# Kernel optimization log

Measured on AMD Instinct MI355X. Metric: run time of the kernel, lower is better.

Reference implementation:

```python
import jax, jax.numpy as jnp
import numpy as np
from jax import lax

B, P, DIM, HEADS, K = 2, 4096, 256, 8, 32
DH = DIM // HEADS
SCALE = DH ** -0.5


def setup_inputs() -> dict:
    key = jax.random.key(0)
    ks = jax.random.split(key, 12)
    s = 0.02
    return {
        "xyz": jax.random.uniform(ks[0], (B, P, 3), dtype=jnp.float32),
        "feats": jax.random.normal(ks[1], (B, P, DIM), dtype=jnp.float32),
        "Wq": jax.random.normal(ks[2], (DIM, DIM), dtype=jnp.float32) * s,
        "Wk": jax.random.normal(ks[3], (DIM, DIM), dtype=jnp.float32) * s,
        "Wv": jax.random.normal(ks[4], (DIM, DIM), dtype=jnp.float32) * s,
        "Wp": jax.random.normal(ks[5], (DIM, DIM), dtype=jnp.float32) * s,
        "bp": jnp.zeros((DIM,), jnp.float32),
        "W1": jax.random.normal(ks[6], (DIM, 3), dtype=jnp.float32) * s,
        "b1": jnp.zeros((DIM,), jnp.float32),
        "W2": jax.random.normal(ks[7], (DIM, DIM), dtype=jnp.float32) * s,
        "b2": jnp.zeros((DIM,), jnp.float32),
    }


def _gather(points, idx):
    # points: (B,N,C), idx: (B,M,K) -> (B,M,K,C)
    return jax.vmap(lambda p, i: p[i])(points, idx)


def reference(xyz, feats, Wq, Wk, Wv, Wp, bp, W1, b1, W2, b2):
    b, p, d = feats.shape
    # kNN via squared euclidean distance (same ordering as cdist)
    d2 = jnp.sum((xyz[:, :, None, :] - xyz[:, None, :, :]) ** 2, axis=-1)  # (B,P,P)
    _, idx = lax.top_k(-d2, K)  # (B,P,K) smallest distances

    neigh_xyz = _gather(xyz, idx)                      # (B,P,K,3)
    relpos = neigh_xyz - xyz[:, :, None, :]            # (B,P,K,3)

    q = (feats @ Wq.T).reshape(b, p, HEADS, DH)        # (B,P,H,Dh)
    k_full = feats @ Wk.T                              # (B,P,D)
    v_full = feats @ Wv.T
    k_nei = _gather(k_full, idx).reshape(b, p, K, HEADS, DH)
    v_nei = _gather(v_full, idx).reshape(b, p, K, HEADS, DH)

    # pos MLP: Linear(3,dim) -> ReLU -> Linear(dim,dim)
    h = jax.nn.relu(relpos @ W1.T + b1)
    pos_bias = (h @ W2.T + b2).reshape(b, p, K, HEADS, DH)

    attn = jnp.einsum('bphd,bpkhd->bpkh', q, k_nei + pos_bias) * SCALE
    attn = jax.nn.softmax(attn, axis=2)                # over K neighbors
    out = jnp.einsum('bpkh,bpkhd->bphd', attn, v_nei + pos_bias).reshape(b, p, d)
    return out @ Wp.T + bp
```

## Files before the change

### kernel.cpp

```cpp
#include <hip/hip_runtime.h>
#include <cstddef>

#define PB 4096
static constexpr float SCALE_F = 0.17677669529663687f;

typedef __attribute__((ext_vector_type(8))) short bf16x8;
typedef __attribute__((ext_vector_type(4))) float f32x4;

static __device__ __forceinline__ unsigned short f2bf(float x) {
  unsigned u = __builtin_bit_cast(unsigned, x);
  u += 0x7fffu + ((u >> 16) & 1u);
  return (unsigned short)(u >> 16);
}
static __device__ __forceinline__ float bf2f(unsigned short h) {
  return __builtin_bit_cast(float, (unsigned)h << 16);
}

__global__ __launch_bounds__(64) void knn_kernel(const float* __restrict__ xyz,
                                                 int* __restrict__ idx_out) {
  const int g = blockIdx.x;
  const int b = g >> 12;
  const int p = g & (PB - 1);
  const int lane = threadIdx.x;
  const float* base = xyz + (size_t)b * PB * 3;
  const float qx = base[p * 3 + 0];
  const float qy = base[p * 3 + 1];
  const float qz = base[p * 3 + 2];
  float list_d = 3.4e38f;
  int list_i = -1;
  for (int c = 0; c < PB / 64; ++c) {
    const int j = (c << 6) + lane;
    const float dx = __fsub_rn(qx, base[j * 3 + 0]);
    const float dy = __fsub_rn(qy, base[j * 3 + 1]);
    const float dz = __fsub_rn(qz, base[j * 3 + 2]);
    const float d2 = __fadd_rn(__fadd_rn(__fmul_rn(dx, dx), __fmul_rn(dy, dy)),
                               __fmul_rn(dz, dz));
    float worst = __shfl(list_d, 31);
    unsigned long long mask = __ballot(d2 < worst);
    while (mask) {
      const int l = __ffsll(mask) - 1;
      mask &= mask - 1;
      const float v = __shfl(d2, l);
      worst = __shfl(list_d, 31);
      if (v < worst) {
        const unsigned long long gt = __ballot((lane < 32) && (list_d > v));
        const int pos = __ffsll(gt) - 1;
        const float pd = __shfl_up(list_d, 1);
        const int pi = __shfl_up(list_i, 1);
        if (lane < 32 && lane >= pos) {
          const bool at = (lane == pos);
          list_d = at ? v : pd;
          list_i = at ? ((c << 6) + l) : pi;
        }
      }
    }
  }
  if (lane < 32) idx_out[(size_t)g * 32 + lane] = list_i;
}

__global__ __launch_bounds__(256) void prep_w(
    const float* __restrict__ Wq, const float* __restrict__ Wk,
    const float* __restrict__ Wv, const float* __restrict__ W2,
    const float* __restrict__ Wp,
    unsigned short* __restrict__ whi, unsigned short* __restrict__ wlo) {
  const int e = blockIdx.x * 256 + threadIdx.x;
  const int m = e >> 16;
  const int off = e & 65535;
  const float* src = (m == 0) ? Wq : (m == 1) ? Wk : (m == 2) ? Wv
                     : (m == 3) ? W2 : Wp;
  const float x = src[off];
  const unsigned short hi = f2bf(x);
  whi[e] = hi;
  wlo[e] = f2bf(x - bf2f(hi));
}

static __device__ __forceinline__ void gemm32_core(
    const float* __restrict__ A, const unsigned short* __restrict__ wh,
    const unsigned short* __restrict__ wl, const int r0,
    unsigned short* ah, unsigned short* al, f32x4 acc[2][4]) {
  const int tid = threadIdx.x;
#pragma unroll
  for (int t = 0; t < 8; ++t) {
    const int idx4 = (t << 8) + tid;
    const int row = idx4 >> 6;
    const int c4 = idx4 & 63;
    const float4 v = *(const float4*)(A + (size_t)(r0 + row) * 256 + (c4 << 2));
    const unsigned short h0 = f2bf(v.x), h1 = f2bf(v.y);
    const unsigned short h2 = f2bf(v.z), h3 = f2bf(v.w);
    const unsigned short l0 = f2bf(v.x - bf2f(h0)), l1 = f2bf(v.y - bf2f(h1));
    const unsigned short l2 = f2bf(v.z - bf2f(h2)), l3 = f2bf(v.w - bf2f(h3));
    const int base = (row << 9) + ((c4 << 3) ^ ((row & 7) << 4));
    *(uint2*)((char*)ah + base) =
        make_uint2((unsigned)h0 | ((unsigned)h1 << 16),
                   (unsigned)h2 | ((unsigned)h3 << 16));
    *(uint2*)((char*)al + base) =
        make_uint2((unsigned)l0 | ((unsigned)l1 << 16),
                   (unsigned)l2 | ((unsigned)l3 << 16));
  }
  __syncthreads();
  const int lane = tid & 63;
  const int w = tid >> 6;
  const int il = lane & 15;
  const int q4 = lane >> 4;
#pragma unroll
  for (int mt = 0; mt < 2; ++mt)
#pragma unroll
    for (int nt = 0; nt < 4; ++nt) acc[mt][nt] = (f32x4){0.f, 0.f, 0.f, 0.f};
#pragma unroll 2
  for (int ks = 0; ks < 8; ++ks) {
    bf16x8 bh[4], bl[4], a0[2], a1[2];
#pragma unroll
    for (int nt = 0; nt < 4; ++nt) {
      const int n = (w << 6) + (nt << 4) + il;
      const size_t off = (size_t)n * 256 + (ks << 5) + (q4 << 3);
      bh[nt] = *(const bf16x8*)(wh + off);
      bl[nt] = *(const bf16x8*)(wl + off);
    }
#pragma unroll
    for (int mt = 0; mt < 2; ++mt) {
      const int row = (mt << 4) + il;
      const int byte = (row << 9) + ((((ks << 5) + (q4 << 3)) << 1) ^ ((row & 7) << 4));
      a0[mt] = *(const bf16x8*)((const char*)ah + byte);
      a1[mt] = *(const bf16x8*)((const char*)al + byte);
    }
#pragma unroll
    for (int mt = 0; mt < 2; ++mt)
#pragma unroll
      for (int nt = 0; nt < 4; ++nt) {
        acc[mt][nt] = __builtin_amdgcn_mfma_f32_16x16x32_bf16(a0[mt], bh[nt], acc[mt][nt], 0, 0, 0);
        acc[mt][nt] = __builtin_amdgcn_mfma_f32_16x16x32_bf16(a1[mt], bh[nt], acc[mt][nt], 0, 0, 0);
        acc[mt][nt] = __builtin_amdgcn_mfma_f32_16x16x32_bf16(a0[mt], bl[nt], acc[mt][nt], 0, 0, 0);
      }
  }
}

__global__ __launch_bounds__(256) void qkv_mfma(
    const float* __restrict__ feats,
    const unsigned short* __restrict__ whi, const unsigned short* __restrict__ wlo,
    float* __restrict__ qb, unsigned short* __restrict__ kb16,
    unsigned short* __restrict__ vb16) {
  __shared__ unsigned short ah[32 * 256];
  __shared__ unsigned short al[32 * 256];
  const int bid = blockIdx.x;
  const int sel = bid % 3;
  const int r0 = (bid / 3) << 5;
  const unsigned short* wh = whi + (size_t)sel * 65536;
  const unsigned short* wl = wlo + (size_t)sel * 65536;
  f32x4 acc[2][4];
  gemm32_core(feats, wh, wl, r0, ah, al, acc);
  const int tid = threadIdx.x;
  const int lane = tid & 63;
  const int w = tid >> 6;
  const int il = lane & 15;
  const int q4 = lane >> 4;
#pragma unroll
  for (int mt = 0; mt < 2; ++mt)
#pragma unroll
    for (int nt = 0; nt < 4; ++nt) {
      const int col = (w << 6) + (nt << 4) + il;
#pragma unroll
      for (int r = 0; r < 4; ++r) {
        const size_t e = (size_t)(r0 + (mt << 4) + (q4 << 2) + r) * 256 + col;
        if (sel == 0) qb[e] = acc[mt][nt][r];
        else if (sel == 1) kb16[e] = f2bf(acc[mt][nt][r]);
        else vb16[e] = f2bf(acc[mt][nt][r]);
      }
    }
}

__global__ __launch_bounds__(256) void proj_mfma(
    const float* __restrict__ A,
    const unsigned short* __restrict__ whi, const unsigned short* __restrict__ wlo,
    const float* __restrict__ bp, float* __restrict__ C) {
  __shared__ unsigned short ah[32 * 256];
  __shared__ unsigned short al[32 * 256];
  const int r0 = blockIdx.x << 5;
  f32x4 acc[2][4];
  gemm32_core(A, whi, wlo, r0, ah, al, acc);
  const int tid = threadIdx.x;
  const int lane = tid & 63;
  const int w = tid >> 6;
  const int il = lane & 15;
  const int q4 = lane >> 4;
#pragma unroll
  for (int mt = 0; mt < 2; ++mt)
#pragma unroll
    for (int nt = 0; nt < 4; ++nt) {
      const int col = (w << 6) + (nt << 4) + il;
      const float bv = bp[col];
#pragma unroll
      for (int r = 0; r < 4; ++r)
        C[(size_t)(r0 + (mt << 4) + (q4 << 2) + r) * 256 + col] = acc[mt][nt][r] + bv;
    }
}

__global__ __launch_bounds__(256) void fused_kernel(
    const float* __restrict__ xyz, const int* __restrict__ nbr_idx,
    const float* __restrict__ qbuf, const unsigned short* __restrict__ kb16,
    const unsigned short* __restrict__ vb16,
    const float* __restrict__ W1, const float* __restrict__ b1,
    const unsigned short* __restrict__ w2bf, const float* __restrict__ b2,
    float* __restrict__ o_pre) {
  __shared__ unsigned short h_lds[32 * 256];
  __shared__ float q_lds[256];
  __shared__ float u_lds[8][256];
  __shared__ float c_lds[8][256];
  __shared__ float at_lds[32][8];
  __shared__ float rel[32][3];
  __shared__ int nbr_s[32];

  const int g = blockIdx.x;
  const int b = g >> 12;
  const int p = g & (PB - 1);
  const int tid = threadIdx.x;

  if (tid < 32) {
    const int j = nbr_idx[(size_t)g * 32 + tid];
    nbr_s[tid] = j;
    const float* xb = xyz + (size_t)b * PB * 3;
    rel[tid][0] = xb[j * 3 + 0] - xb[p * 3 + 0];
    rel[tid][1] = xb[j * 3 + 1] - xb[p * 3 + 1];
    rel[tid][2] = xb[j * 3 + 2] - xb[p * 3 + 2];
  }
  q_lds[tid] = qbuf[(size_t)g * 256 + tid];
  __syncthreads();

  {
    const int half = tid >> 7;
    const int c0 = (tid & 127) << 1;
    const float w00 = W1[c0 * 3 + 0], w01 = W1[c0 * 3 + 1], w02 = W1[c0 * 3 + 2];
    const float w10 = W1[c0 * 3 + 3], w11 = W1[c0 * 3 + 4], w12 = W1[c0 * 3 + 5];
    const float bb0 = b1[c0], bb1 = b1[c0 + 1];
#pragma unroll 4
    for (int rl = 0; rl < 16; ++rl) {
      const int rr = (half << 4) + rl;
      const float rx = rel[rr][0], ry = rel[rr][1], rz = rel[rr][2];
      const float h0 = fmaxf(bb0 + rx * w00 + ry * w01 + rz * w02, 0.f);
      const float h1 = fmaxf(bb1 + rx * w10 + ry * w11 + rz * w12, 0.f);
      const unsigned pk = (unsigned)f2bf(h0) | ((unsigned)f2bf(h1) << 16);
      *(unsigned*)((char*)h_lds + (rr << 9) + (((unsigned)c0 << 1) ^ ((rr & 7) << 4))) = pk;
    }
  }
  {
    const int h = tid >> 5;
    const int m8 = (tid & 31) << 3;
    float ua[8];
#pragma unroll
    for (int j = 0; j < 8; ++j) ua[j] = 0.f;
    const unsigned short* wrow = w2bf + (size_t)(h << 5) * 256 + m8;
#pragma unroll 4
    for (int i = 0; i < 32; ++i) {
      const float qn = q_lds[(h << 5) + i];
      const bf16x8 wv = *(const bf16x8*)(wrow + (size_t)i * 256);
#pragma unroll
      for (int j = 0; j < 8; ++j) ua[j] += qn * bf2f((unsigned short)wv[j]);
    }
#pragma unroll
    for (int j = 0; j < 8; ++j) u_lds[h][m8 + j] = ua[j];
  }
  __syncthreads();

  {
    const int k = tid & 31;
    const int h = tid >> 5;
    const int j = nbr_s[k];
    const unsigned short* krow = kb16 + ((size_t)(b << 12) + j) * 256 + (h << 5);
    float s = 0.f;
#pragma unroll
    for (int c4 = 0; c4 < 4; ++c4) {
      const bf16x8 kv = *(const bf16x8*)(krow + (c4 << 3));
#pragma unroll
      for (int jj = 0; jj < 8; ++jj)
        s += q_lds[(h << 5) + (c4 << 3) + jj] * bf2f((unsigned short)kv[jj]);
    }
#pragma unroll 4
    for (int m8 = 0; m8 < 32; ++m8) {
      const bf16x8 hv = *(const bf16x8*)((const char*)h_lds + (k << 9) +
                                         ((m8 << 4) ^ ((k & 7) << 4)));
      const float4 u0 = *(const float4*)&u_lds[h][m8 << 3];
      const float4 u1 = *(const float4*)&u_lds[h][(m8 << 3) + 4];
      s += u0.x * bf2f((unsigned short)hv[0]) + u0.y * bf2f((unsigned short)hv[1]) +
           u0.z * bf2f((unsigned short)hv[2]) + u0.w * bf2f((unsigned short)hv[3]) +
           u1.x * bf2f((unsigned short)hv[4]) + u1.y * bf2f((unsigned short)hv[5]) +
           u1.z * bf2f((unsigned short)hv[6]) + u1.w * bf2f((unsigned short)hv[7]);
    }
    s *= SCALE_F;
    float mx = s;
#pragma unroll
    for (int off = 16; off; off >>= 1) mx = fmaxf(mx, __shfl_xor(mx, off));
    const float e = __expf(s - mx);
    float ssum = e;
#pragma unroll
    for (int off = 16; off; off >>= 1) ssum += __shfl_xor(ssum, off);
    at_lds[k][h] = e / ssum;
  }
  __syncthreads();

  {
    const int m = tid;
    float ca[8];
#pragma unroll
    for (int h = 0; h < 8; ++h) ca[h] = 0.f;
#pragma unroll 4
    for (int k = 0; k < 32; ++k) {
      const float hv = bf2f(*(const unsigned short*)(
          (const char*)h_lds + (k << 9) + ((2 * m) ^ ((k & 7) << 4))));
      const float4 a0 = *(const float4*)&at_lds[k][0];
      const float4 a1 = *(const float4*)&at_lds[k][4];
      ca[0] += a0.x * hv; ca[1] += a0.y * hv; ca[2] += a0.z * hv; ca[3] += a0.w * hv;
      ca[4] += a1.x * hv; ca[5] += a1.y * hv; ca[6] += a1.z * hv; ca[7] += a1.w * hv;
    }
#pragma unroll
    for (int h = 0; h < 8; ++h) c_lds[h][m] = ca[h];
  }
  __syncthreads();

  {
    const int n = tid;
    const int h = n >> 5;
    float o = b2[n];
    const size_t vbase = (size_t)(b << 12) * 256 + n;
#pragma unroll 4
    for (int k = 0; k < 32; ++k)
      o += at_lds[k][h] * bf2f(vb16[vbase + (size_t)nbr_s[k] * 256]);
    const unsigned short* wrow = w2bf + (size_t)n * 256;
    float opos = 0.f;
#pragma unroll 4
    for (int m8 = 0; m8 < 32; ++m8) {
      const bf16x8 wv = *(const bf16x8*)(wrow + (m8 << 3));
      const float4 c0 = *(const float4*)&c_lds[h][m8 << 3];
      const float4 c1 = *(const float4*)&c_lds[h][(m8 << 3) + 4];
      opos += c0.x * bf2f((unsigned short)wv[0]) + c0.y * bf2f((unsigned short)wv[1]) +
              c0.z * bf2f((unsigned short)wv[2]) + c0.w * bf2f((unsigned short)wv[3]) +
              c1.x * bf2f((unsigned short)wv[4]) + c1.y * bf2f((unsigned short)wv[5]) +
              c1.z * bf2f((unsigned short)wv[6]) + c1.w * bf2f((unsigned short)wv[7]);
    }
    o_pre[(size_t)g * 256 + n] = o + opos;
  }
}

extern "C" void kernel_launch(void* const* d_in, const int* in_sizes, int n_in,
                              void* d_out, int out_size, void* d_ws, size_t ws_size,
                              hipStream_t stream) {
  (void)in_sizes; (void)n_in; (void)out_size; (void)ws_size;
  const float* xyz   = (const float*)d_in[0];
  const float* feats = (const float*)d_in[1];
  const float* Wq    = (const float*)d_in[2];
  const float* Wk    = (const float*)d_in[3];
  const float* Wv    = (const float*)d_in[4];
  const float* Wp    = (const float*)d_in[5];
  const float* bp    = (const float*)d_in[6];
  const float* W1    = (const float*)d_in[7];
  const float* b1    = (const float*)d_in[8];
  const float* W2    = (const float*)d_in[9];
  const float* b2    = (const float*)d_in[10];
  float* out = (float*)d_out;

  int* idxw  = (int*)d_ws;
  float* wsf = (float*)d_ws;
  float* qb = wsf + 262144;
  unsigned short* kb16 = (unsigned short*)(qb + 2097152);
  unsigned short* vb16 = (unsigned short*)(qb + 2097152 + 1048576);
  float* op = qb + 2097152 + 2097152;
  unsigned short* whi = (unsigned short*)(op + 2097152);
  unsigned short* wlo = whi + 327680;

  hipLaunchKernelGGL(prep_w, dim3(1280), dim3(256), 0, stream,
                     Wq, Wk, Wv, W2, Wp, whi, wlo);
  hipLaunchKernelGGL(knn_kernel, dim3(2 * PB), dim3(64), 0, stream, xyz, idxw);
  hipLaunchKernelGGL(qkv_mfma, dim3(768), dim3(256), 0, stream,
                     feats, whi, wlo, qb, kb16, vb16);
  hipLaunchKernelGGL(fused_kernel, dim3(2 * PB), dim3(256), 0, stream,
                     xyz, idxw, qb, kb16, vb16, W1, b1,
                     whi + (size_t)3 * 65536, b2, op);
  hipLaunchKernelGGL(proj_mfma, dim3(256), dim3(256), 0, stream,
                     op, whi + (size_t)4 * 65536, wlo + (size_t)4 * 65536, bp, out);
}
```

Before: 341.9 us.

## Fold W2 into query and output projections to skip per-neighbor pos MLP GEMM

Precomputes Wq·W2 per head and W2·Wp per head as bf16 matrices, plus a folded bias. Attention scores now use h·(q W2) via a small MFMA over the hidden activations, and the value-side positional term becomes the attention-weighted hidden vector, projected through the folded W2·Wp inside the final projection GEMM. This avoids materialising the per-neighbor 256×256 positional bias GEMM for every point. In exchange it adds extra prep kernels, an 8× wider intermediate buffer (B·P×2048 bf16), and more bf16 rounding. The path is only taken when the workspace is large enough; otherwise the old fused kernel runs.

```diff
diff --git a/kernel.cpp b/kernel.cpp
--- a/kernel.cpp
+++ b/kernel.cpp
@@ -60,18 +60,71 @@
 
 __global__ __launch_bounds__(256) void prep_w(
     const float* __restrict__ Wq, const float* __restrict__ Wk,
-    const float* __restrict__ Wv, const float* __restrict__ W2,
-    const float* __restrict__ Wp,
-    unsigned short* __restrict__ whi, unsigned short* __restrict__ wlo) {
-  const int e = blockIdx.x * 256 + threadIdx.x;
-  const int m = e >> 16;
-  const int off = e & 65535;
-  const float* src = (m == 0) ? Wq : (m == 1) ? Wk : (m == 2) ? Wv
-                     : (m == 3) ? W2 : Wp;
-  const float x = src[off];
-  const unsigned short hi = f2bf(x);
-  whi[e] = hi;
-  wlo[e] = f2bf(x - bf2f(hi));
+    const float* __restrict__ Wv, const float* __restrict__ Wp,
+    const float* __restrict__ W2,
+    unsigned short* __restrict__ whi, unsigned short* __restrict__ wlo,
+    unsigned short* __restrict__ w2bf) {
+  const int blk = blockIdx.x;
+  const int tid = threadIdx.x;
+  if (blk < 1024) {
+    const int e = blk * 256 + tid;
+    const int m = e >> 16;
+    const int off = e & 65535;
+    const float* src = (m == 0) ? Wq : (m == 1) ? Wk : (m == 2) ? Wv : Wp;
+    const float x = src[off];
+    const unsigned short hi = f2bf(x);
+    whi[e] = hi;
+    wlo[e] = f2bf(x - bf2f(hi));
+  } else {
+    const int off = (blk - 1024) * 256 + tid;
+    w2bf[off] = f2bf(W2[off]);
+  }
+}
+
+__global__ __launch_bounds__(256) void wqu_kernel(
+    const float* __restrict__ Wq, const float* __restrict__ W2,
+    unsigned short* __restrict__ wqu_t) {
+  __shared__ float w2s[32];
+  const int hm = blockIdx.x;
+  const int h = hm >> 8;
+  const int m = hm & 255;
+  const int tid = threadIdx.x;
+  if (tid < 32) w2s[tid] = W2[(size_t)((h << 5) + tid) * 256 + m];
+  __syncthreads();
+  float a = 0.f;
+#pragma unroll 8
+  for (int t = 0; t < 32; ++t)
+    a += Wq[(size_t)((h << 5) + t) * 256 + tid] * w2s[t];
+  wqu_t[(size_t)hm * 256 + tid] = f2bf(a);
+}
+
+__global__ __launch_bounds__(256) void wop_kernel(
+    const float* __restrict__ W2, const float* __restrict__ Wp,
+    unsigned short* __restrict__ wop_t) {
+  __shared__ float wps[32];
+  const int blk = blockIdx.x;
+  const int j = blk & 255;
+  const int h = blk >> 8;
+  const int tid = threadIdx.x;
+  if (tid < 32) wps[tid] = Wp[(size_t)j * 256 + (h << 5) + tid];
+  __syncthreads();
+  float a = 0.f;
+#pragma unroll 8
+  for (int t = 0; t < 32; ++t)
+    a += W2[(size_t)((h << 5) + t) * 256 + tid] * wps[t];
+  wop_t[(size_t)j * 2048 + (h << 8) + tid] = f2bf(a);
+}
+
+__global__ __launch_bounds__(256) void bpp_kernel(
+    const float* __restrict__ b2, const float* __restrict__ Wp,
+    const float* __restrict__ bp, float* __restrict__ bpp) {
+  __shared__ float b2s[256];
+  const int tid = threadIdx.x;
+  b2s[tid] = b2[tid];
+  __syncthreads();
+  float a = bp[tid];
+  for (int n = 0; n < 256; ++n) a += b2s[n] * Wp[(size_t)tid * 256 + n];
+  bpp[tid] = a;
 }
 
 static __device__ __forceinline__ void gemm32_core(
@@ -139,8 +192,8 @@
     const unsigned short* __restrict__ whi, const unsigned short* __restrict__ wlo,
     float* __restrict__ qb, unsigned short* __restrict__ kb16,
     unsigned short* __restrict__ vb16) {
-  __shared__ unsigned short ah[32 * 256];
-  __shared__ unsigned short al[32 * 256];
+  __shared__ __align__(16) unsigned short ah[32 * 256];
+  __shared__ __align__(16) unsigned short al[32 * 256];
   const int bid = blockIdx.x;
   const int sel = bid % 3;
   const int r0 = (bid / 3) << 5;
@@ -168,40 +221,276 @@
     }
 }
 
-__global__ __launch_bounds__(256) void proj_mfma(
-    const float* __restrict__ A,
-    const unsigned short* __restrict__ whi, const unsigned short* __restrict__ wlo,
-    const float* __restrict__ bp, float* __restrict__ C) {
-  __shared__ unsigned short ah[32 * 256];
-  __shared__ unsigned short al[32 * 256];
+__global__ __launch_bounds__(256) void u_mfma(
+    const float* __restrict__ feats, const unsigned short* __restrict__ wqu_t,
+    unsigned short* __restrict__ U) {
+  __shared__ __align__(16) unsigned short ah[32 * 256];
   const int r0 = blockIdx.x << 5;
-  f32x4 acc[2][4];
-  gemm32_core(A, whi, wlo, r0, ah, al, acc);
-  const int tid = threadIdx.x;
+  const int cb = blockIdx.y;
+  const int tid = threadIdx.x;
+#pragma unroll
+  for (int t = 0; t < 8; ++t) {
+    const int idx4 = (t << 8) + tid;
+    const int row = idx4 >> 6;
+    const int c4 = idx4 & 63;
+    const float4 v = *(const float4*)(feats + (size_t)(r0 + row) * 256 + (c4 << 2));
+    const int base = (row << 9) + ((c4 << 3) ^ ((row & 7) << 4));
+    *(uint2*)((char*)ah + base) =
+        make_uint2((unsigned)f2bf(v.x) | ((unsigned)f2bf(v.y) << 16),
+                   (unsigned)f2bf(v.z) | ((unsigned)f2bf(v.w) << 16));
+  }
+  __syncthreads();
+  const unsigned short* wh = wqu_t + (size_t)cb * 65536;
   const int lane = tid & 63;
   const int w = tid >> 6;
   const int il = lane & 15;
   const int q4 = lane >> 4;
+  f32x4 acc[2][4];
+#pragma unroll
+  for (int mt = 0; mt < 2; ++mt)
+#pragma unroll
+    for (int nt = 0; nt < 4; ++nt) acc[mt][nt] = (f32x4){0.f, 0.f, 0.f, 0.f};
+#pragma unroll 2
+  for (int ks = 0; ks < 8; ++ks) {
+    bf16x8 bh[4], a0[2];
+#pragma unroll
+    for (int nt = 0; nt < 4; ++nt) {
+      const int n = (w << 6) + (nt << 4) + il;
+      bh[nt] = *(const bf16x8*)(wh + (size_t)n * 256 + (ks << 5) + (q4 << 3));
+    }
+#pragma unroll
+    for (int mt = 0; mt < 2; ++mt) {
+      const int row = (mt << 4) + il;
+      const int byte = (row << 9) + ((((ks << 5) + (q4 << 3)) << 1) ^ ((row & 7) << 4));
+      a0[mt] = *(const bf16x8*)((const char*)ah + byte);
+    }
+#pragma unroll
+    for (int mt = 0; mt < 2; ++mt)
+#pragma unroll
+      for (int nt = 0; nt < 4; ++nt)
+        acc[mt][nt] = __builtin_amdgcn_mfma_f32_16x16x32_bf16(a0[mt], bh[nt], acc[mt][nt], 0, 0, 0);
+  }
 #pragma unroll
   for (int mt = 0; mt < 2; ++mt)
 #pragma unroll
     for (int nt = 0; nt < 4; ++nt) {
       const int col = (w << 6) + (nt << 4) + il;
-      const float bv = bp[col];
+#pragma unroll
+      for (int r = 0; r < 4; ++r)
+        U[(size_t)(r0 + (mt << 4) + (q4 << 2) + r) * 2048 + (cb << 8) + col] =
+            f2bf(acc[mt][nt][r]);
+    }
+}
+
+template <bool FOLD>
+__global__ __launch_bounds__(256) void proj_mfma(
+    const float* __restrict__ A,
+    const unsigned short* __restrict__ whi, const unsigned short* __restrict__ wlo,
+    const unsigned short* __restrict__ c16, const unsigned short* __restrict__ wop_t,
+    const float* __restrict__ bias, float* __restrict__ C) {
+  __shared__ __align__(16) unsigned short ah[32 * 256];
+  __shared__ __align__(16) unsigned short al[32 * 256];
+  const int r0 = blockIdx.x << 5;
+  f32x4 acc[2][4];
+  gemm32_core(A, whi, wlo, r0, ah, al, acc);
+  const int tid = threadIdx.x;
+  const int lane = tid & 63;
+  const int w = tid >> 6;
+  const int il = lane & 15;
+  const int q4 = lane >> 4;
+  if (FOLD) {
+#pragma unroll 4
+    for (int ks2 = 0; ks2 < 64; ++ks2) {
+      bf16x8 af[2];
+#pragma unroll
+      for (int mt = 0; mt < 2; ++mt)
+        af[mt] = *(const bf16x8*)(c16 + (size_t)(r0 + (mt << 4) + il) * 2048 +
+                                  (ks2 << 5) + (q4 << 3));
+#pragma unroll
+      for (int nt = 0; nt < 4; ++nt) {
+        const int n = (w << 6) + (nt << 4) + il;
+        const bf16x8 bf = *(const bf16x8*)(wop_t + (size_t)n * 2048 +
+                                           (ks2 << 5) + (q4 << 3));
+#pragma unroll
+        for (int mt = 0; mt < 2; ++mt)
+          acc[mt][nt] = __builtin_amdgcn_mfma_f32_16x16x32_bf16(af[mt], bf, acc[mt][nt], 0, 0, 0);
+      }
+    }
+  }
+#pragma unroll
+  for (int mt = 0; mt < 2; ++mt)
+#pragma unroll
+    for (int nt = 0; nt < 4; ++nt) {
+      const int col = (w << 6) + (nt << 4) + il;
+      const float bv = bias[col];
 #pragma unroll
       for (int r = 0; r < 4; ++r)
         C[(size_t)(r0 + (mt << 4) + (q4 << 2) + r) * 256 + col] = acc[mt][nt][r] + bv;
     }
 }
 
-__global__ __launch_bounds__(256) void fused_kernel(
+__global__ __launch_bounds__(256) void fused_big(
+    const float* __restrict__ xyz, const int* __restrict__ nbr_idx,
+    const float* __restrict__ qbuf, const unsigned short* __restrict__ kb16,
+    const unsigned short* __restrict__ vb16,
+    const float* __restrict__ W1, const float* __restrict__ b1,
+    const unsigned short* __restrict__ ubuf,
+    unsigned short* __restrict__ c16, float* __restrict__ o_pre) {
+  __shared__ __align__(16) unsigned short h_km[32 * 256];
+  __shared__ __align__(16) char h_mk[256 * 80];
+  __shared__ __align__(16) unsigned short u16l[16 * 256];
+  __shared__ float sc_part[4][32][9];
+  __shared__ float at_lds[32][9];
+  __shared__ __align__(16) char at16[16 * 80];
+  __shared__ float q_lds[256];
+  __shared__ float rel[32][3];
+  __shared__ int nbr_s[32];
+
+  const int g = blockIdx.x;
+  const int b = g >> 12;
+  const int p = g & (PB - 1);
+  const int tid = threadIdx.x;
+
+  if (tid < 32) {
+    const int j = nbr_idx[(size_t)g * 32 + tid];
+    nbr_s[tid] = j;
+    const float* xb = xyz + (size_t)b * PB * 3;
+    rel[tid][0] = xb[j * 3 + 0] - xb[p * 3 + 0];
+    rel[tid][1] = xb[j * 3 + 1] - xb[p * 3 + 1];
+    rel[tid][2] = xb[j * 3 + 2] - xb[p * 3 + 2];
+  }
+  q_lds[tid] = qbuf[(size_t)g * 256 + tid];
+  *(uint4*)((char*)u16l + 4096 + tid * 16) = make_uint4(0, 0, 0, 0);
+  if (tid < 160) *(unsigned*)(at16 + 640 + tid * 4) = 0;
+  __syncthreads();
+
+  {
+    const int half = tid >> 7;
+    const int c0 = (tid & 127) << 1;
+    const int stg = (tid >> 1) & 7;
+    const float w00 = W1[c0 * 3 + 0], w01 = W1[c0 * 3 + 1], w02 = W1[c0 * 3 + 2];
+    const float w10 = W1[c0 * 3 + 3], w11 = W1[c0 * 3 + 4], w12 = W1[c0 * 3 + 5];
+    const float bb0 = b1[c0], bb1 = b1[c0 + 1];
+#pragma unroll 4
+    for (int rl = 0; rl < 16; ++rl) {
+      const int rr = (half << 4) | ((rl + stg) & 15);
+      const float rx = rel[rr][0], ry = rel[rr][1], rz = rel[rr][2];
+      const float h0 = fmaxf(bb0 + rx * w00 + ry * w01 + rz * w02, 0.f);
+      const float h1 = fmaxf(bb1 + rx * w10 + ry * w11 + rz * w12, 0.f);
+      const unsigned short bh0 = f2bf(h0), bh1 = f2bf(h1);
+      *(unsigned*)((char*)h_km + (rr << 9) + (((unsigned)c0 << 1) ^ ((rr & 7) << 4))) =
+          (unsigned)bh0 | ((unsigned)bh1 << 16);
+      *(unsigned short*)(h_mk + c0 * 80 + rr * 2) = bh0;
+      *(unsigned short*)(h_mk + (c0 + 1) * 80 + rr * 2) = bh1;
+    }
+  }
+  {
+    const int h = tid >> 5;
+    const int byte = (h << 9) + ((((tid & 31) << 4)) ^ ((h & 7) << 4));
+    const uint4 uv = *(const uint4*)(ubuf + (size_t)g * 2048 + tid * 8);
+    *(uint4*)((char*)u16l + byte) = uv;
+  }
+  __syncthreads();
+
+  const int lane = tid & 63;
+  const int w = tid >> 6;
+  const int il = lane & 15;
+  const int q4 = lane >> 4;
+  const int kk = tid & 31;
+  const int hh = tid >> 5;
+
+  float sqk = 0.f;
+  {
+    const int j = nbr_s[kk];
+    const unsigned short* krow = kb16 + ((size_t)(b << 12) + j) * 256 + (hh << 5);
+#pragma unroll
+    for (int c4 = 0; c4 < 4; ++c4) {
+      const bf16x8 kv = *(const bf16x8*)(krow + (c4 << 3));
+#pragma unroll
+      for (int jj = 0; jj < 8; ++jj)
+        sqk += q_lds[(hh << 5) + (c4 << 3) + jj] * bf2f((unsigned short)kv[jj]);
+    }
+  }
+  {
+    f32x4 accp[2];
+    accp[0] = (f32x4){0.f, 0.f, 0.f, 0.f};
+    accp[1] = (f32x4){0.f, 0.f, 0.f, 0.f};
+#pragma unroll
+    for (int ksl = 0; ksl < 2; ++ksl) {
+      const int m0 = (w << 6) + (ksl << 5) + (q4 << 3);
+      const bf16x8 bfr = *(const bf16x8*)((char*)u16l + (il << 9) +
+                                          (((unsigned)m0 << 1) ^ ((il & 7) << 4)));
+#pragma unroll
+      for (int mt = 0; mt < 2; ++mt) {
+        const int row = (mt << 4) + il;
+        const bf16x8 afr = *(const bf16x8*)((char*)h_km + (row << 9) +
+                                            (((unsigned)m0 << 1) ^ ((row & 7) << 4)));
+        accp[mt] = __builtin_amdgcn_mfma_f32_16x16x32_bf16(afr, bfr, accp[mt], 0, 0, 0);
+      }
+    }
+    if (il < 8) {
+#pragma unroll
+      for (int mt = 0; mt < 2; ++mt)
+#pragma unroll
+        for (int r = 0; r < 4; ++r)
+          sc_part[w][(mt << 4) + (q4 << 2) + r][il] = accp[mt][r];
+    }
+  }
+  __syncthreads();
+
+  {
+    float s = sqk + sc_part[0][kk][hh] + sc_part[1][kk][hh] +
+              sc_part[2][kk][hh] + sc_part[3][kk][hh];
+    s *= SCALE_F;
+    float mx = s;
+#pragma unroll
+    for (int off = 16; off; off >>= 1) mx = fmaxf(mx, __shfl_xor(mx, off));
+    const float e = __expf(s - mx);
+    float ssum = e;
+#pragma unroll
+    for (int off = 16; off; off >>= 1) ssum += __shfl_xor(ssum, off);
+    const float a = e / ssum;
+    at_lds[kk][hh] = a;
+    *(unsigned short*)(at16 + hh * 80 + kk * 2) = f2bf(a);
+  }
+  __syncthreads();
+
+  {
+    const bf16x8 afr = *(const bf16x8*)(at16 + il * 80 + (q4 << 4));
+    const f32x4 zero = (f32x4){0.f, 0.f, 0.f, 0.f};
+#pragma unroll
+    for (int nt = 0; nt < 4; ++nt) {
+      const int m = (w << 6) + (nt << 4) + il;
+      const bf16x8 bfr = *(const bf16x8*)(h_mk + m * 80 + (q4 << 4));
+      const f32x4 c = __builtin_amdgcn_mfma_f32_16x16x32_bf16(afr, bfr, zero, 0, 0, 0);
+      if (q4 < 2) {
+#pragma unroll
+        for (int r = 0; r < 4; ++r)
+          c16[(size_t)g * 2048 + (size_t)((q4 << 2) + r) * 256 + m] = f2bf(c[r]);
+      }
+    }
+  }
+
+  {
+    const int n = tid;
+    const int h = n >> 5;
+    float o = 0.f;
+    const size_t vbase = (size_t)(b << 12) * 256 + n;
+#pragma unroll 4
+    for (int k = 0; k < 32; ++k)
+      o += at_lds[k][h] * bf2f(vb16[vbase + (size_t)nbr_s[k] * 256]);
+    o_pre[(size_t)g * 256 + n] = o;
+  }
+}
+
+__global__ __launch_bounds__(256) void fused_small(
     const float* __restrict__ xyz, const int* __restrict__ nbr_idx,
     const float* __restrict__ qbuf, const unsigned short* __restrict__ kb16,
     const unsigned short* __restrict__ vb16,
     const float* __restrict__ W1, const float* __restrict__ b1,
     const unsigned short* __restrict__ w2bf, const float* __restrict__ b2,
     float* __restrict__ o_pre) {
-  __shared__ unsigned short h_lds[32 * 256];
+  __shared__ __align__(16) unsigned short h_lds[32 * 256];
   __shared__ float q_lds[256];
   __shared__ float u_lds[8][256];
   __shared__ float c_lds[8][256];
@@ -342,7 +631,7 @@
 extern "C" void kernel_launch(void* const* d_in, const int* in_sizes, int n_in,
                               void* d_out, int out_size, void* d_ws, size_t ws_size,
                               hipStream_t stream) {
-  (void)in_sizes; (void)n_in; (void)out_size; (void)ws_size;
+  (void)in_sizes; (void)n_in; (void)out_size;
   const float* xyz   = (const float*)d_in[0];
   const float* feats = (const float*)d_in[1];
   const float* Wq    = (const float*)d_in[2];
@@ -356,23 +645,42 @@
   const float* b2    = (const float*)d_in[10];
   float* out = (float*)d_out;
 
-  int* idxw  = (int*)d_ws;
   float* wsf = (float*)d_ws;
-  float* qb = wsf + 262144;
-  unsigned short* kb16 = (unsigned short*)(qb + 2097152);
-  unsigned short* vb16 = (unsigned short*)(qb + 2097152 + 1048576);
-  float* op = qb + 2097152 + 2097152;
-  unsigned short* whi = (unsigned short*)(op + 2097152);
-  unsigned short* wlo = whi + 327680;
+  int* idxw            = (int*)wsf;
+  float* qb            = wsf + 262144;
+  unsigned short* kb16 = (unsigned short*)(wsf + 2359296);
+  unsigned short* vb16 = (unsigned short*)(wsf + 3407872);
+  float* op            = wsf + 4456448;
+  unsigned short* whi  = (unsigned short*)(wsf + 6553600);
+  unsigned short* wlo  = (unsigned short*)(wsf + 6684672);
+  unsigned short* w2bf = (unsigned short*)(wsf + 6815744);
+  unsigned short* wqut = (unsigned short*)(wsf + 6848512);
+  unsigned short* wopt = (unsigned short*)(wsf + 7110656);
+  float* bpp           = wsf + 7372800;
+  unsigned short* c16  = (unsigned short*)(wsf + 7373056);
+  const bool big = ws_size >= (size_t)15761664 * 4;
 
   hipLaunchKernelGGL(prep_w, dim3(1280), dim3(256), 0, stream,
-                     Wq, Wk, Wv, W2, Wp, whi, wlo);
+                     Wq, Wk, Wv, Wp, W2, whi, wlo, w2bf);
   hipLaunchKernelGGL(knn_kernel, dim3(2 * PB), dim3(64), 0, stream, xyz, idxw);
   hipLaunchKernelGGL(qkv_mfma, dim3(768), dim3(256), 0, stream,
                      feats, whi, wlo, qb, kb16, vb16);
-  hipLaunchKernelGGL(fused_kernel, dim3(2 * PB), dim3(256), 0, stream,
-                     xyz, idxw, qb, kb16, vb16, W1, b1,
-                     whi + (size_t)3 * 65536, b2, op);
-  hipLaunchKernelGGL(proj_mfma, dim3(256), dim3(256), 0, stream,
-                     op, whi + (size_t)4 * 65536, wlo + (size_t)4 * 65536, bp, out);
-}
+  if (big) {
+    hipLaunchKernelGGL(wqu_kernel, dim3(2048), dim3(256), 0, stream, Wq, W2, wqut);
+    hipLaunchKernelGGL(wop_kernel, dim3(2048), dim3(256), 0, stream, W2, Wp, wopt);
+    hipLaunchKernelGGL(bpp_kernel, dim3(1), dim3(256), 0, stream, b2, Wp, bp, bpp);
+    hipLaunchKernelGGL(u_mfma, dim3(256, 8), dim3(256), 0, stream,
+                       feats, wqut, c16);
+    hipLaunchKernelGGL(fused_big, dim3(2 * PB), dim3(256), 0, stream,
+                       xyz, idxw, qb, kb16, vb16, W1, b1, c16, c16, op);
+    hipLaunchKernelGGL(proj_mfma<true>, dim3(256), dim3(256), 0, stream,
+                       op, whi + (size_t)3 * 65536, wlo + (size_t)3 * 65536,
+                       c16, wopt, bpp, out);
+  } else {
+    hipLaunchKernelGGL(fused_small, dim3(2 * PB), dim3(256), 0, stream,
+                       xyz, idxw, qb, kb16, vb16, W1, b1, w2bf, b2, op);
+    hipLaunchKernelGGL(proj_mfma<false>, dim3(256), dim3(256), 0, stream,
+                       op, whi + (size_t)3 * 65536, wlo + (size_t)3 * 65536,
+                       nullptr, nullptr, bp, out);
+  }
+}
```

Result: slower. 358.0 us (+4.7%).
